# Optimization experiments

Measured on AMD Instinct MI355X. Metric: run time of the kernel, lower is better.

Reference implementation:

```python
import jax, jax.numpy as jnp
import numpy as np

ALPHA = 0.25
GAMMA = 2.0
EPS = 1e-8


def setup_inputs() -> dict:
    key = jax.random.key(0)
    k1, k2 = jax.random.split(key)
    B, V, T = 2048, 32000, 20
    src = jax.random.uniform(k1, (B, V), dtype=jnp.float32)
    tgt = jax.random.randint(k2, (B, T), 0, V, dtype=jnp.int64)
    return {"src": src, "tgt": tgt}


def reference(src, tgt):
    B, V = src.shape
    # Ragged one-hot target build: scatter 1.0 at (row, token_id).
    rows = jnp.arange(B)[:, None]  # [B, 1] broadcast against tgt [B, T]
    gloss_targets = jnp.zeros((B, V), dtype=jnp.float32).at[rows, tgt].set(1.0)

    prob = jnp.clip(src.astype(jnp.float32), EPS, 1.0 - EPS)
    bce = -(gloss_targets * jnp.log(prob) + (1.0 - gloss_targets) * jnp.log(1.0 - prob))
    p_t = prob * gloss_targets + (1.0 - prob) * (1.0 - gloss_targets)
    alpha_t = ALPHA * gloss_targets + (1.0 - ALPHA) * (1.0 - gloss_targets)
    focal_weight = alpha_t * jnp.power(1.0 - p_t, GAMMA)
    loss = focal_weight * bce
    return loss.sum()
```

## Files before the change

kernel.cpp:

```cpp
#include <hip/hip_runtime.h>

#define NT 256
#define NB 2048
#define B_ 2048
#define V_ 32000
#define T_ 20

__device__ __forceinline__ float clip_p(float p) {
    return fmaxf(p, 1e-8f);
}

__device__ __forceinline__ float loss_t0(float pc) {
    float om = 1.0f - pc;
    return -0.51986038542f * pc * pc * __builtin_amdgcn_logf(om);
}

__device__ __forceinline__ float loss_t1(float pc) {
    float om = 1.0f - pc;
    return -0.17328679514f * om * om * __builtin_amdgcn_logf(pc);
}

__device__ __forceinline__ double block_reduce_f64(double v) {
    #pragma unroll
    for (int off = 32; off > 0; off >>= 1) v += __shfl_down(v, off, 64);
    __shared__ double lds[NT / 64];
    int lane = threadIdx.x & 63;
    int wid  = threadIdx.x >> 6;
    if (lane == 0) lds[wid] = v;
    __syncthreads();
    double s = 0.0;
    if (threadIdx.x == 0) {
        #pragma unroll
        for (int w = 0; w < NT / 64; ++w) s += lds[w];
    }
    return s;
}

__global__ __launch_bounds__(NT) void focal_fused(const float* __restrict__ src,
                                                  const int* __restrict__ tgt,
                                                  double* __restrict__ part) {
    double acc = 0.0;

    if (threadIdx.x < T_) {
        int row = blockIdx.x;
        const int* trow = tgt + row * T_;
        int t   = threadIdx.x;
        int idx = trow[t];
        bool first = true;
        for (int u = 0; u < t; ++u)
            if (trow[u] == idx) first = false;
        if (first && idx >= 0 && idx < V_) {
            float pc = clip_p(src[(long)row * V_ + idx]);
            acc = (double)(loss_t1(pc) - loss_t0(pc));
        }
    }

    const long n4 = (long)B_ * V_ / 4;
    const long stride = (long)NB * NT;
    long i = (long)blockIdx.x * NT + threadIdx.x;
    const float4* s4 = (const float4*)src;
    for (; i < n4; i += stride) {
        float4 v = s4[i];
        float a = loss_t0(clip_p(v.x)) + loss_t0(clip_p(v.y)) +
                  loss_t0(clip_p(v.z)) + loss_t0(clip_p(v.w));
        acc += (double)a;
    }

    double s = block_reduce_f64(acc);
    if (threadIdx.x == 0) part[blockIdx.x] = s;
}

__global__ __launch_bounds__(NT) void focal_final(const double* __restrict__ part,
                                                  float* __restrict__ out) {
    double acc = 0.0;
    for (int i = threadIdx.x; i < NB; i += NT) acc += part[i];
    double s = block_reduce_f64(acc);
    if (threadIdx.x == 0) out[0] = (float)s;
}

extern "C" void kernel_launch(void* const* d_in, const int* in_sizes, int n_in,
                              void* d_out, int out_size, void* d_ws, size_t ws_size,
                              hipStream_t stream) {
    const float* src = (const float*)d_in[0];
    const int*   tgt = (const int*)d_in[1];
    float*       out = (float*)d_out;
    double*      part = (double*)d_ws;

    focal_fused<<<NB, NT, 0, stream>>>(src, tgt, part);
    focal_final<<<1, NT, 0, stream>>>(part, out);
}
```

Before: 350.2 us.

## Fuse final reduction into single cooperative kernel with grid sync

```diff
diff --git a/kernel.cpp b/kernel.cpp
--- a/kernel.cpp
+++ b/kernel.cpp
@@ -1,7 +1,10 @@
 #include <hip/hip_runtime.h>
+#include <hip/hip_cooperative_groups.h>
+
+namespace cg = cooperative_groups;
 
 #define NT 256
-#define NB 2048
+#define NB 1024
 #define B_ 2048
 #define V_ 32000
 #define T_ 20
@@ -20,6 +23,11 @@
     return -0.17328679514f * om * om * __builtin_amdgcn_logf(pc);
 }
 
+__device__ __forceinline__ float loss4_t0(float4 v) {
+    return loss_t0(clip_p(v.x)) + loss_t0(clip_p(v.y)) +
+           loss_t0(clip_p(v.z)) + loss_t0(clip_p(v.w));
+}
+
 __device__ __forceinline__ double block_reduce_f64(double v) {
     #pragma unroll
     for (int off = 32; off > 0; off >>= 1) v += __shfl_down(v, off, 64);
@@ -36,15 +44,16 @@
     return s;
 }
 
-__global__ __launch_bounds__(NT) void focal_fused(const float* __restrict__ src,
-                                                  const int* __restrict__ tgt,
-                                                  double* __restrict__ part) {
+__global__ __launch_bounds__(NT, 4) void focal_all(const float* __restrict__ src,
+                                                   const int* __restrict__ tgt,
+                                                   double* __restrict__ part,
+                                                   float* __restrict__ out) {
     double acc = 0.0;
 
-    if (threadIdx.x < T_) {
-        int row = blockIdx.x;
+    if (threadIdx.x < 2 * T_) {
+        int row = blockIdx.x * 2 + (threadIdx.x / T_);
+        int t   = threadIdx.x % T_;
         const int* trow = tgt + row * T_;
-        int t   = threadIdx.x;
         int idx = trow[t];
         bool first = true;
         for (int u = 0; u < t; ++u)
@@ -59,23 +68,25 @@
     const long stride = (long)NB * NT;
     long i = (long)blockIdx.x * NT + threadIdx.x;
     const float4* s4 = (const float4*)src;
-    for (; i < n4; i += stride) {
-        float4 v = s4[i];
-        float a = loss_t0(clip_p(v.x)) + loss_t0(clip_p(v.y)) +
-                  loss_t0(clip_p(v.z)) + loss_t0(clip_p(v.w));
-        acc += (double)a;
+    for (; i + stride < n4; i += 2 * stride) {
+        float4 v0 = s4[i];
+        float4 v1 = s4[i + stride];
+        acc += (double)loss4_t0(v0);
+        acc += (double)loss4_t0(v1);
     }
+    if (i < n4) acc += (double)loss4_t0(s4[i]);
 
     double s = block_reduce_f64(acc);
     if (threadIdx.x == 0) part[blockIdx.x] = s;
-}
 
-__global__ __launch_bounds__(NT) void focal_final(const double* __restrict__ part,
-                                                  float* __restrict__ out) {
-    double acc = 0.0;
-    for (int i = threadIdx.x; i < NB; i += NT) acc += part[i];
-    double s = block_reduce_f64(acc);
-    if (threadIdx.x == 0) out[0] = (float)s;
+    cg::this_grid().sync();
+
+    if (blockIdx.x == 0) {
+        double a2 = 0.0;
+        for (int k = threadIdx.x; k < NB; k += NT) a2 += part[k];
+        double s2 = block_reduce_f64(a2);
+        if (threadIdx.x == 0) out[0] = (float)s2;
+    }
 }
 
 extern "C" void kernel_launch(void* const* d_in, const int* in_sizes, int n_in,
@@ -86,6 +97,6 @@
     float*       out = (float*)d_out;
     double*      part = (double*)d_ws;
 
-    focal_fused<<<NB, NT, 0, stream>>>(src, tgt, part);
-    focal_final<<<1, NT, 0, stream>>>(part, out);
+    void* args[] = { (void*)&src, (void*)&tgt, (void*)&part, (void*)&out };
+    hipLaunchCooperativeKernel((void*)focal_all, dim3(NB), dim3(NT), args, 0, stream);
 }
```

Result: slower. 454.9 us (+29.9%).
